# Performance work log

Hardware: AMD Instinct MI355X
Metric: run time of the kernel (lower is better)

The kernel has to match this reference:

```python
import jax, jax.numpy as jnp
import numpy as np

V, E, B, C = 10000, 128, 16, 128
N_REL = 8

def setup_inputs() -> dict:
    key = jax.random.key(0)
    k1, k2, k3, k4, k5 = jax.random.split(key, 5)
    src = jax.random.randint(k1, (B, C), 0, V, dtype=jnp.int32)
    src_embed = jax.random.normal(k2, (B, C, E), dtype=jnp.float32)
    embed_weight = jax.random.normal(k3, (V, E), dtype=jnp.float32)
    edge_matrix = jax.random.uniform(k4, (V, V), dtype=jnp.float32)
    relation_matrix = jax.random.randint(k5, (V, V), 0, 9, dtype=jnp.int32)
    return {"src": src, "src_embed": src_embed, "embed_weight": embed_weight,
            "edge_matrix": edge_matrix, "relation_matrix": relation_matrix}

def reference(src, src_embed, embed_weight, edge_matrix, relation_matrix):
    # base scores against full vocab: [B, C, V]
    base = jnp.einsum('bce,ve->bcv', src_embed, embed_weight)
    # gather the rows of both tables once: [B, C, V]
    edge_rows = edge_matrix[src]
    rel_rows = relation_matrix[src]
    concept_embeddings = []
    scores = []
    for i in range(N_REL):
        # ((relation_matrix == i+1) * edge_matrix)[src] > 0, gathered form
        mask = (jnp.where(rel_rows == i + 1, edge_rows, 0.0) > 0).astype(base.dtype)
        concept_weights = mask * base                     # [B, C, V]
        attn = jax.nn.softmax(concept_weights, axis=2)     # softmax over full vocab
        ce = jnp.einsum('bcv,ve->bce', attn, embed_weight) # [B, C, E]
        concept_embeddings.append(ce)
        scores.append(jnp.sum(src_embed * ce, axis=2, keepdims=True))
    scores = jnp.concatenate(scores, axis=2)               # [B, C, 8]
    weights = jax.nn.softmax(scores, axis=2)
    final = jnp.zeros_like(src_embed)
    for i in range(N_REL):
        final = final + weights[:, :, i:i + 1] * concept_embeddings[i]
    return final
```

## Files before the change

### kernel.cpp

```cpp
#include <hip/hip_runtime.h>

#define VV 10000
#define EE 128
#define NROWS 2048
#define KS 32

typedef unsigned short u16;
using short8 = __attribute__((ext_vector_type(8))) short;
using f32x4  = __attribute__((ext_vector_type(4))) float;

__device__ __forceinline__ u16 f2bf(float x) {
    unsigned u = __float_as_uint(x);
    return (u16)((u + 0x7fffu + ((u >> 16) & 1u)) >> 16);
}
__device__ __forceinline__ float bf2f(u16 h) {
    return __uint_as_float(((unsigned)h) << 16);
}

__global__ __launch_bounds__(256) void k0_prep(
    const float* __restrict__ SE,
    const float* __restrict__ W,
    u16* __restrict__ SEh, u16* __restrict__ SEl,
    u16* __restrict__ Wh,  u16* __restrict__ Wl,
    u16* __restrict__ WTh, u16* __restrict__ WTl)
{
    const int u = blockIdx.x * 256 + threadIdx.x;
    float x[8];
    u16 *dh, *dl;

    if (u < 32768) {
        int fid = u >> 6, l = u & 63;
        int nf = fid >> 2, kt = fid & 3;
        int row = nf * 16 + (l & 15);
        int k0 = kt * 32 + (l >> 4) * 8;
        const float* p = SE + row * EE + k0;
        float4 a = *(const float4*)p, b = *(const float4*)(p + 4);
        x[0]=a.x; x[1]=a.y; x[2]=a.z; x[3]=a.w;
        x[4]=b.x; x[5]=b.y; x[6]=b.z; x[7]=b.w;
        dh = SEh + u * 8; dl = SEl + u * 8;
    } else if (u < 192768) {
        int u2 = u - 32768;
        int fid = u2 >> 6, l = u2 & 63;
        int vf = fid >> 2, kt = fid & 3;
        int row = vf * 16 + (l & 15);
        int k0 = kt * 32 + (l >> 4) * 8;
        const float* p = W + row * EE + k0;
        float4 a = *(const float4*)p, b = *(const float4*)(p + 4);
        x[0]=a.x; x[1]=a.y; x[2]=a.z; x[3]=a.w;
        x[4]=b.x; x[5]=b.y; x[6]=b.z; x[7]=b.w;
        dh = Wh + u2 * 8; dl = Wl + u2 * 8;
    } else {
        int u3 = u - 192768;
        int fid = u3 >> 6, l = u3 & 63;
        int ef = fid / 313, kc = fid - ef * 313;
        int e  = ef * 16 + (l & 15);
        int k8 = kc * 32 + (l >> 4) * 8;
        if (k8 < VV) {
            #pragma unroll
            for (int i = 0; i < 8; i++) x[i] = W[(k8 + i) * EE + e];
        } else {
            #pragma unroll
            for (int i = 0; i < 8; i++) x[i] = 0.f;
        }
        dh = WTh + u3 * 8; dl = WTl + u3 * 8;
    }

    short8 hv, lv;
    #pragma unroll
    for (int i = 0; i < 8; i++) {
        u16 hb = f2bf(x[i]);
        hv[i] = (short)hb;
        lv[i] = (short)f2bf(x[i] - bf2f(hb));
    }
    *(short8*)dh = hv;
    *(short8*)dl = lv;
}

__global__ __launch_bounds__(256) void k1_mfma(
    const u16* __restrict__ SEh, const u16* __restrict__ SEl,
    const u16* __restrict__ Wh,  const u16* __restrict__ Wl,
    float* __restrict__ base)
{
    const int tid = threadIdx.x;
    const int l = tid & 63, wv = tid >> 6;
    const int wn = wv >> 1, wq = wv & 1;
    const int vt = blockIdx.x, nt = blockIdx.y;
    const int nf0 = nt * 4 + wn * 2;
    const int vf0 = vt * 8 + wq * 4;

    f32x4 acc[2][4];
    #pragma unroll
    for (int i = 0; i < 2; i++)
        #pragma unroll
        for (int j = 0; j < 4; j++)
            acc[i][j] = (f32x4){0.f, 0.f, 0.f, 0.f};

    #pragma unroll
    for (int kt = 0; kt < 4; ++kt) {
        short8 ah[2], al[2];
        #pragma unroll
        for (int i = 0; i < 2; ++i) {
            int off = (((nf0 + i) * 4 + kt) * 64 + l) * 8;
            ah[i] = *(const short8*)(SEh + off);
            al[i] = *(const short8*)(SEl + off);
        }
        #pragma unroll
        for (int j = 0; j < 4; ++j) {
            int vf = vf0 + j;
            short8 bh = {0,0,0,0,0,0,0,0};
            short8 bl = {0,0,0,0,0,0,0,0};
            if (vf < 625) {
                int off = ((vf * 4 + kt) * 64 + l) * 8;
                bh = *(const short8*)(Wh + off);
                bl = *(const short8*)(Wl + off);
            }
            #pragma unroll
            for (int i = 0; i < 2; ++i) {
                acc[i][j] = __builtin_amdgcn_mfma_f32_16x16x32_bf16(ah[i], bh, acc[i][j], 0, 0, 0);
                acc[i][j] = __builtin_amdgcn_mfma_f32_16x16x32_bf16(ah[i], bl, acc[i][j], 0, 0, 0);
                acc[i][j] = __builtin_amdgcn_mfma_f32_16x16x32_bf16(al[i], bh, acc[i][j], 0, 0, 0);
            }
        }
    }

    const int c = l & 15, r0 = (l >> 4) * 4;
    #pragma unroll
    for (int j = 0; j < 4; ++j) {
        int vf = vf0 + j;
        if (vf >= 625) continue;
        int v = vf * 16 + c;
        #pragma unroll
        for (int i = 0; i < 2; ++i) {
            int n = (nf0 + i) * 16 + r0;
            #pragma unroll
            for (int r = 0; r < 4; ++r)
                base[(n + r) * VV + v] = acc[i][j][r];
        }
    }
}

__global__ __launch_bounds__(256) void k2_stats(
    const int*   __restrict__ src,
    const float* __restrict__ edge,
    const int*   __restrict__ rel,
    float* __restrict__ baseA)
{
    __shared__ float seb[VV];
    __shared__ unsigned char srb[VV];
    __shared__ float wred[33][4];
    __shared__ float fin[33];
    __shared__ float cvals[12];

    const int n = blockIdx.x;
    const int tid = threadIdx.x;
    const int lane = tid & 63;
    const int wv = tid >> 6;
    const int s = src[n];
    const float4* brow4 = (const float4*)(baseA + (long long)n * VV);
    const float4* erow4 = (const float4*)(edge + (long long)s * VV);
    const int4*   rrow4 = (const int4*)(rel + (long long)s * VV);

    float accv[33];
    #pragma unroll
    for (int i = 0; i < 33; i++) accv[i] = 0.f;

    for (int v4 = tid; v4 < VV / 4; v4 += 256) {
        float4 b = brow4[v4];
        float4 e = erow4[v4];
        int4   r = rrow4[v4];
        float bb[4] = {b.x, b.y, b.z, b.w};
        float ee[4] = {e.x, e.y, e.z, e.w};
        int   rr[4] = {r.x, r.y, r.z, r.w};
        #pragma unroll
        for (int c = 0; c < 4; c++) {
            int rb = (rr[c] >= 1 && rr[c] <= 8 && ee[c] > 0.f) ? rr[c] : 0;
            float bc = bb[c];
            float eb = __expf(bc);
            float beb = bc * eb;
            seb[v4 * 4 + c] = eb;
            srb[v4 * 4 + c] = (unsigned char)rb;
            accv[0] += bc;
            #pragma unroll
            for (int q = 0; q < 8; q++) {
                float m = (rb == q + 1) ? 1.f : 0.f;
                accv[1 + q]  += m;
                accv[9 + q]  = fmaf(m, bc,  accv[9 + q]);
                accv[17 + q] = fmaf(m, eb,  accv[17 + q]);
                accv[25 + q] = fmaf(m, beb, accv[25 + q]);
            }
        }
    }

    #pragma unroll
    for (int i = 0; i < 33; i++) {
        float x = accv[i];
        #pragma unroll
        for (int off = 32; off > 0; off >>= 1) x += __shfl_xor(x, off, 64);
        if (lane == 0) wred[i][wv] = x;
    }
    __syncthreads();
    if (tid < 33)
        fin[tid] = wred[tid][0] + wred[tid][1] + wred[tid][2] + wred[tid][3];
    __syncthreads();

    if (tid == 0) {
        float sumbase = fin[0];
        float sc[8], Z[8];
        float smax = -1e30f;
        #pragma unroll
        for (int q = 0; q < 8; q++) {
            Z[q]  = ((float)VV - fin[1 + q]) + fin[17 + q];
            sc[q] = (sumbase - fin[9 + q] + fin[25 + q]) / Z[q];
            smax = fmaxf(smax, sc[q]);
        }
        float wsum = 0.f, wq[8];
        #pragma unroll
        for (int q = 0; q < 8; q++) { wq[q] = __expf(sc[q] - smax); wsum += wq[q]; }
        float Kc = 0.f;
        #pragma unroll
        for (int q = 0; q < 8; q++) {
            float c = (wq[q] / wsum) / Z[q];
            cvals[1 + q] = c;
            Kc += c;
        }
        cvals[0] = 0.f;
        cvals[9] = Kc;
    }
    __syncthreads();

    const float Kc = cvals[9];
    float4* broww = (float4*)(baseA + (long long)n * VV);
    for (int v4 = tid; v4 < VV / 4; v4 += 256) {
        float o[4];
        #pragma unroll
        for (int c = 0; c < 4; c++) {
            float eb = seb[v4 * 4 + c];
            float cc = cvals[srb[v4 * 4 + c]];
            o[c] = fmaf(cc, eb - 1.f, Kc);
        }
        broww[v4] = make_float4(o[0], o[1], o[2], o[3]);
    }
}

__global__ __launch_bounds__(256) void k3_mfma(
    const float* __restrict__ A,
    const u16* __restrict__ WTh, const u16* __restrict__ WTl,
    float* __restrict__ part)
{
    const int tid = threadIdx.x;
    const int l = tid & 63, wv = tid >> 6;
    const int mt = blockIdx.x, ks = blockIdx.y;
    const int mf0 = mt * 8 + wv * 2;
    const int g = l >> 4, rr_ = l & 15;

    f32x4 acc[2][8];
    #pragma unroll
    for (int i = 0; i < 2; i++)
        #pragma unroll
        for (int j = 0; j < 8; j++)
            acc[i][j] = (f32x4){0.f, 0.f, 0.f, 0.f};

    for (int kc = ks; kc < 313; kc += KS) {
        int k8 = kc * 32 + g * 8;
        short8 ah[2], al[2];
        #pragma unroll
        for (int i = 0; i < 2; ++i) {
            float x[8];
            if (k8 < VV) {
                const float* p = A + ((mf0 + i) * 16 + rr_) * VV + k8;
                float4 a = *(const float4*)p, b = *(const float4*)(p + 4);
                x[0]=a.x; x[1]=a.y; x[2]=a.z; x[3]=a.w;
                x[4]=b.x; x[5]=b.y; x[6]=b.z; x[7]=b.w;
            } else {
                #pragma unroll
                for (int q = 0; q < 8; q++) x[q] = 0.f;
            }
            #pragma unroll
            for (int q = 0; q < 8; q++) {
                u16 hb = f2bf(x[q]);
                ah[i][q] = (short)hb;
                al[i][q] = (short)f2bf(x[q] - bf2f(hb));
            }
        }
        #pragma unroll
        for (int j = 0; j < 8; ++j) {
            int off = ((j * 313 + kc) * 64 + l) * 8;
            short8 bh = *(const short8*)(WTh + off);
            short8 bl = *(const short8*)(WTl + off);
            #pragma unroll
            for (int i = 0; i < 2; ++i) {
                acc[i][j] = __builtin_amdgcn_mfma_f32_16x16x32_bf16(ah[i], bh, acc[i][j], 0, 0, 0);
                acc[i][j] = __builtin_amdgcn_mfma_f32_16x16x32_bf16(ah[i], bl, acc[i][j], 0, 0, 0);
                acc[i][j] = __builtin_amdgcn_mfma_f32_16x16x32_bf16(al[i], bh, acc[i][j], 0, 0, 0);
            }
        }
    }

    float* pp = part + (long long)ks * NROWS * EE;
    const int c = l & 15, r0 = g * 4;
    #pragma unroll
    for (int i = 0; i < 2; ++i) {
        #pragma unroll
        for (int j = 0; j < 8; ++j) {
            int e = j * 16 + c;
            int m = (mf0 + i) * 16 + r0;
            #pragma unroll
            for (int r = 0; r < 4; ++r)
                pp[(m + r) * EE + e] = acc[i][j][r];
        }
    }
}

__global__ __launch_bounds__(256) void k4_reduce(
    const float* __restrict__ part, float* __restrict__ out)
{
    int idx = blockIdx.x * 256 + threadIdx.x;
    const float4* p = (const float4*)part;
    const int stride = NROWS * EE / 4;
    float4 s = p[idx];
    #pragma unroll
    for (int k = 1; k < KS; k++) {
        float4 t = p[idx + k * stride];
        s.x += t.x; s.y += t.y; s.z += t.z; s.w += t.w;
    }
    ((float4*)out)[idx] = s;
}

extern "C" void kernel_launch(void* const* d_in, const int* in_sizes, int n_in,
                              void* d_out, int out_size, void* d_ws, size_t ws_size,
                              hipStream_t stream) {
    const int*   src  = (const int*)  d_in[0];
    const float* SE   = (const float*)d_in[1];
    const float* W    = (const float*)d_in[2];
    const float* edge = (const float*)d_in[3];
    const int*   rel  = (const int*)  d_in[4];
    float* out  = (float*)d_out;

    float* base = (float*)d_ws;
    float* part = base + (long long)NROWS * VV;
    u16* SEh = (u16*)(part + (long long)KS * NROWS * EE);
    u16* SEl = SEh + 262144;
    u16* Wh  = SEl + 262144;
    u16* Wl  = Wh  + 1280000;
    u16* WTh = Wl  + 1280000;
    u16* WTl = WTh + 1282048;

    k0_prep<<<dim3(1379), 256, 0, stream>>>(SE, W, SEh, SEl, Wh, Wl, WTh, WTl);
    k1_mfma<<<dim3(79, 32), 256, 0, stream>>>(SEh, SEl, Wh, Wl, base);
    k2_stats<<<dim3(NROWS), 256, 0, stream>>>(src, edge, rel, base);
    k3_mfma<<<dim3(16, KS), 256, 0, stream>>>(base, WTh, WTl, part);
    k4_reduce<<<dim3(256), 256, 0, stream>>>(part, out);
}
```

Baseline: 738.5 us.

## Keep stats row data in registers, contiguous K-split and retile matmul kernels

k2_stats stops staging exp values and relation bytes in about 50KB of shared memory. It keeps them in per-thread register arrays (packed relation codes) and adds a launch bound so more blocks can be resident. k3 now gives each wave one 16-row tile instead of two, doubling the grid. Each K-split also takes a contiguous chunk of k-steps instead of a strided one. k1 swaps grid axes so consecutive blocks share the same row tile and vary the vocab tile. The trade-offs are higher register pressure in k2 and less reuse of the W operand in k3.

```diff
diff --git a/kernel.cpp b/kernel.cpp
--- a/kernel.cpp
+++ b/kernel.cpp
@@ -84,7 +84,7 @@
     const int tid = threadIdx.x;
     const int l = tid & 63, wv = tid >> 6;
     const int wn = wv >> 1, wq = wv & 1;
-    const int vt = blockIdx.x, nt = blockIdx.y;
+    const int vt = blockIdx.y, nt = blockIdx.x;
     const int nf0 = nt * 4 + wn * 2;
     const int vf0 = vt * 8 + wq * 4;
 
@@ -139,14 +139,12 @@
     }
 }
 
-__global__ __launch_bounds__(256) void k2_stats(
+__global__ __launch_bounds__(256, 4) void k2_stats(
     const int*   __restrict__ src,
     const float* __restrict__ edge,
     const int*   __restrict__ rel,
     float* __restrict__ baseA)
 {
-    __shared__ float seb[VV];
-    __shared__ unsigned char srb[VV];
     __shared__ float wred[33][4];
     __shared__ float fin[33];
     __shared__ float cvals[12];
@@ -164,31 +162,43 @@
     #pragma unroll
     for (int i = 0; i < 33; i++) accv[i] = 0.f;
 
-    for (int v4 = tid; v4 < VV / 4; v4 += 256) {
-        float4 b = brow4[v4];
-        float4 e = erow4[v4];
-        int4   r = rrow4[v4];
-        float bb[4] = {b.x, b.y, b.z, b.w};
-        float ee[4] = {e.x, e.y, e.z, e.w};
-        int   rr[4] = {r.x, r.y, r.z, r.w};
-        #pragma unroll
-        for (int c = 0; c < 4; c++) {
-            int rb = (rr[c] >= 1 && rr[c] <= 8 && ee[c] > 0.f) ? rr[c] : 0;
-            float bc = bb[c];
-            float eb = __expf(bc);
-            float beb = bc * eb;
-            seb[v4 * 4 + c] = eb;
-            srb[v4 * 4 + c] = (unsigned char)rb;
-            accv[0] += bc;
-            #pragma unroll
-            for (int q = 0; q < 8; q++) {
-                float m = (rb == q + 1) ? 1.f : 0.f;
-                accv[1 + q]  += m;
-                accv[9 + q]  = fmaf(m, bc,  accv[9 + q]);
-                accv[17 + q] = fmaf(m, eb,  accv[17 + q]);
-                accv[25 + q] = fmaf(m, beb, accv[25 + q]);
-            }
-        }
+    float    ebr[10][4];
+    unsigned srp[10];
+
+    #pragma unroll
+    for (int it = 0; it < 10; ++it) {
+        int v4 = tid + it * 256;
+        unsigned pk = 0u;
+        if (v4 < VV / 4) {
+            float4 b = brow4[v4];
+            float4 e = erow4[v4];
+            int4   r = rrow4[v4];
+            float bb[4] = {b.x, b.y, b.z, b.w};
+            float ee[4] = {e.x, e.y, e.z, e.w};
+            int   rr[4] = {r.x, r.y, r.z, r.w};
+            #pragma unroll
+            for (int c = 0; c < 4; c++) {
+                int rb = (rr[c] >= 1 && rr[c] <= 8 && ee[c] > 0.f) ? rr[c] : 0;
+                float bc = bb[c];
+                float eb = __expf(bc);
+                float beb = bc * eb;
+                ebr[it][c] = eb;
+                pk |= ((unsigned)rb) << (8 * c);
+                accv[0] += bc;
+                #pragma unroll
+                for (int q = 0; q < 8; q++) {
+                    float m = (rb == q + 1) ? 1.f : 0.f;
+                    accv[1 + q]  += m;
+                    accv[9 + q]  = fmaf(m, bc,  accv[9 + q]);
+                    accv[17 + q] = fmaf(m, eb,  accv[17 + q]);
+                    accv[25 + q] = fmaf(m, beb, accv[25 + q]);
+                }
+            }
+        } else {
+            #pragma unroll
+            for (int c = 0; c < 4; c++) ebr[it][c] = 1.f;
+        }
+        srp[it] = pk;
     }
 
     #pragma unroll
@@ -230,15 +240,20 @@
 
     const float Kc = cvals[9];
     float4* broww = (float4*)(baseA + (long long)n * VV);
-    for (int v4 = tid; v4 < VV / 4; v4 += 256) {
-        float o[4];
-        #pragma unroll
-        for (int c = 0; c < 4; c++) {
-            float eb = seb[v4 * 4 + c];
-            float cc = cvals[srb[v4 * 4 + c]];
-            o[c] = fmaf(cc, eb - 1.f, Kc);
-        }
-        broww[v4] = make_float4(o[0], o[1], o[2], o[3]);
+    #pragma unroll
+    for (int it = 0; it < 10; ++it) {
+        int v4 = tid + it * 256;
+        if (v4 < VV / 4) {
+            unsigned pk = srp[it];
+            float o[4];
+            #pragma unroll
+            for (int c = 0; c < 4; c++) {
+                float eb = ebr[it][c];
+                float cc = cvals[(pk >> (8 * c)) & 255u];
+                o[c] = fmaf(cc, eb - 1.f, Kc);
+            }
+            broww[v4] = make_float4(o[0], o[1], o[2], o[3]);
+        }
     }
 }
 
@@ -250,24 +265,25 @@
     const int tid = threadIdx.x;
     const int l = tid & 63, wv = tid >> 6;
     const int mt = blockIdx.x, ks = blockIdx.y;
-    const int mf0 = mt * 8 + wv * 2;
+    const int mf = mt * 4 + wv;
     const int g = l >> 4, rr_ = l & 15;
-
-    f32x4 acc[2][8];
-    #pragma unroll
-    for (int i = 0; i < 2; i++)
-        #pragma unroll
-        for (int j = 0; j < 8; j++)
-            acc[i][j] = (f32x4){0.f, 0.f, 0.f, 0.f};
-
-    for (int kc = ks; kc < 313; kc += KS) {
+    const int kc0 = (313 * ks) / KS;
+    const int kc1 = (313 * (ks + 1)) / KS;
+
+    f32x4 acc[8];
+    #pragma unroll
+    for (int j = 0; j < 8; j++) acc[j] = (f32x4){0.f, 0.f, 0.f, 0.f};
+
+    const float* arow = A + (long long)(mf * 16 + rr_) * VV;
+
+    #pragma unroll 2
+    for (int kc = kc0; kc < kc1; ++kc) {
         int k8 = kc * 32 + g * 8;
-        short8 ah[2], al[2];
-        #pragma unroll
-        for (int i = 0; i < 2; ++i) {
+        short8 ah, al;
+        {
             float x[8];
             if (k8 < VV) {
-                const float* p = A + ((mf0 + i) * 16 + rr_) * VV + k8;
+                const float* p = arow + k8;
                 float4 a = *(const float4*)p, b = *(const float4*)(p + 4);
                 x[0]=a.x; x[1]=a.y; x[2]=a.z; x[3]=a.w;
                 x[4]=b.x; x[5]=b.y; x[6]=b.z; x[7]=b.w;
@@ -278,8 +294,8 @@
             #pragma unroll
             for (int q = 0; q < 8; q++) {
                 u16 hb = f2bf(x[q]);
-                ah[i][q] = (short)hb;
-                al[i][q] = (short)f2bf(x[q] - bf2f(hb));
+                ah[q] = (short)hb;
+                al[q] = (short)f2bf(x[q] - bf2f(hb));
             }
         }
         #pragma unroll
@@ -287,27 +303,21 @@
             int off = ((j * 313 + kc) * 64 + l) * 8;
             short8 bh = *(const short8*)(WTh + off);
             short8 bl = *(const short8*)(WTl + off);
-            #pragma unroll
-            for (int i = 0; i < 2; ++i) {
-                acc[i][j] = __builtin_amdgcn_mfma_f32_16x16x32_bf16(ah[i], bh, acc[i][j], 0, 0, 0);
-                acc[i][j] = __builtin_amdgcn_mfma_f32_16x16x32_bf16(ah[i], bl, acc[i][j], 0, 0, 0);
-                acc[i][j] = __builtin_amdgcn_mfma_f32_16x16x32_bf16(al[i], bh, acc[i][j], 0, 0, 0);
-            }
+            acc[j] = __builtin_amdgcn_mfma_f32_16x16x32_bf16(ah, bh, acc[j], 0, 0, 0);
+            acc[j] = __builtin_amdgcn_mfma_f32_16x16x32_bf16(ah, bl, acc[j], 0, 0, 0);
+            acc[j] = __builtin_amdgcn_mfma_f32_16x16x32_bf16(al, bh, acc[j], 0, 0, 0);
         }
     }
 
     float* pp = part + (long long)ks * NROWS * EE;
     const int c = l & 15, r0 = g * 4;
     #pragma unroll
-    for (int i = 0; i < 2; ++i) {
-        #pragma unroll
-        for (int j = 0; j < 8; ++j) {
-            int e = j * 16 + c;
-            int m = (mf0 + i) * 16 + r0;
-            #pragma unroll
-            for (int r = 0; r < 4; ++r)
-                pp[(m + r) * EE + e] = acc[i][j][r];
-        }
+    for (int j = 0; j < 8; ++j) {
+        int e = j * 16 + c;
+        int m = mf * 16 + r0;
+        #pragma unroll
+        for (int r = 0; r < 4; ++r)
+            pp[(m + r) * EE + e] = acc[j][r];
     }
 }
 
@@ -346,8 +356,8 @@
     u16* WTl = WTh + 1282048;
 
     k0_prep<<<dim3(1379), 256, 0, stream>>>(SE, W, SEh, SEl, Wh, Wl, WTh, WTl);
-    k1_mfma<<<dim3(79, 32), 256, 0, stream>>>(SEh, SEl, Wh, Wl, base);
+    k1_mfma<<<dim3(32, 79), 256, 0, stream>>>(SEh, SEl, Wh, Wl, base);
     k2_stats<<<dim3(NROWS), 256, 0, stream>>>(src, edge, rel, base);
-    k3_mfma<<<dim3(16, KS), 256, 0, stream>>>(base, WTh, WTl, part);
+    k3_mfma<<<dim3(32, KS), 256, 0, stream>>>(base, WTh, WTl, part);
     k4_reduce<<<dim3(256), 256, 0, stream>>>(part, out);
 }
```

After: 757.2 us. 2.5% more time.

## Fuse attention-weight construction into the second GEMM using packed relation codes

Applied to the files above, without the earlier changes.

k2 no longer writes the rewritten attention matrix back over base. It emits packed 4-bit relation codes per element plus 10 per-row coefficients, and k3 rebuilds the weights on the fly from base, exp, and a shared-memory coefficient lookup. This drops one full write and re-read of the 2048x10000 float matrix and frees about 50KB of shared memory in k2, at the cost of recomputing exp inside the GEMM loop. k3 is also retiled to 64 rows by 4 E-fragments per wave with contiguous K ranges per split, and k1's grid axes are swapped to change block ordering.

```diff
diff --git a/kernel.cpp b/kernel.cpp
--- a/kernel.cpp
+++ b/kernel.cpp
@@ -4,6 +4,7 @@
 #define EE 128
 #define NROWS 2048
 #define KS 32
+#define RBSTRIDE 5120
 
 typedef unsigned short u16;
 using short8 = __attribute__((ext_vector_type(8))) short;
@@ -84,7 +85,7 @@
     const int tid = threadIdx.x;
     const int l = tid & 63, wv = tid >> 6;
     const int wn = wv >> 1, wq = wv & 1;
-    const int vt = blockIdx.x, nt = blockIdx.y;
+    const int vt = blockIdx.y, nt = blockIdx.x;
     const int nf0 = nt * 4 + wn * 2;
     const int vf0 = vt * 8 + wq * 4;
 
@@ -143,13 +144,12 @@
     const int*   __restrict__ src,
     const float* __restrict__ edge,
     const int*   __restrict__ rel,
-    float* __restrict__ baseA)
-{
-    __shared__ float seb[VV];
-    __shared__ unsigned char srb[VV];
+    const float* __restrict__ baseA,
+    unsigned char* __restrict__ rb4,
+    float* __restrict__ cG)
+{
     __shared__ float wred[33][4];
     __shared__ float fin[33];
-    __shared__ float cvals[12];
 
     const int n = blockIdx.x;
     const int tid = threadIdx.x;
@@ -159,6 +159,7 @@
     const float4* brow4 = (const float4*)(baseA + (long long)n * VV);
     const float4* erow4 = (const float4*)(edge + (long long)s * VV);
     const int4*   rrow4 = (const int4*)(rel + (long long)s * VV);
+    unsigned short* crow = (unsigned short*)(rb4 + (long long)n * RBSTRIDE);
 
     float accv[33];
     #pragma unroll
@@ -171,14 +172,14 @@
         float bb[4] = {b.x, b.y, b.z, b.w};
         float ee[4] = {e.x, e.y, e.z, e.w};
         int   rr[4] = {r.x, r.y, r.z, r.w};
+        unsigned pk = 0u;
         #pragma unroll
         for (int c = 0; c < 4; c++) {
             int rb = (rr[c] >= 1 && rr[c] <= 8 && ee[c] > 0.f) ? rr[c] : 0;
             float bc = bb[c];
             float eb = __expf(bc);
             float beb = bc * eb;
-            seb[v4 * 4 + c] = eb;
-            srb[v4 * 4 + c] = (unsigned char)rb;
+            pk |= ((unsigned)rb) << (4 * c);
             accv[0] += bc;
             #pragma unroll
             for (int q = 0; q < 8; q++) {
@@ -189,6 +190,7 @@
                 accv[25 + q] = fmaf(m, beb, accv[25 + q]);
             }
         }
+        crow[v4] = (unsigned short)pk;
     }
 
     #pragma unroll
@@ -217,60 +219,77 @@
         #pragma unroll
         for (int q = 0; q < 8; q++) { wq[q] = __expf(sc[q] - smax); wsum += wq[q]; }
         float Kc = 0.f;
+        float* cg = cG + n * 10;
         #pragma unroll
         for (int q = 0; q < 8; q++) {
             float c = (wq[q] / wsum) / Z[q];
-            cvals[1 + q] = c;
+            cg[1 + q] = c;
             Kc += c;
         }
-        cvals[0] = 0.f;
-        cvals[9] = Kc;
-    }
-    __syncthreads();
-
-    const float Kc = cvals[9];
-    float4* broww = (float4*)(baseA + (long long)n * VV);
-    for (int v4 = tid; v4 < VV / 4; v4 += 256) {
-        float o[4];
-        #pragma unroll
-        for (int c = 0; c < 4; c++) {
-            float eb = seb[v4 * 4 + c];
-            float cc = cvals[srb[v4 * 4 + c]];
-            o[c] = fmaf(cc, eb - 1.f, Kc);
-        }
-        broww[v4] = make_float4(o[0], o[1], o[2], o[3]);
+        cg[0] = 0.f;
+        cg[9] = Kc;
     }
 }
 
 __global__ __launch_bounds__(256) void k3_mfma(
-    const float* __restrict__ A,
+    const float* __restrict__ baseA,
+    const unsigned char* __restrict__ rb4,
+    const float* __restrict__ cG,
     const u16* __restrict__ WTh, const u16* __restrict__ WTl,
     float* __restrict__ part)
 {
+    __shared__ float cvt[64][10];
+
     const int tid = threadIdx.x;
     const int l = tid & 63, wv = tid >> 6;
+    const int wm = wv >> 1, we = wv & 1;
     const int mt = blockIdx.x, ks = blockIdx.y;
-    const int mf0 = mt * 8 + wv * 2;
     const int g = l >> 4, rr_ = l & 15;
-
-    f32x4 acc[2][8];
+    const int kc0 = (313 * ks) / KS;
+    const int kc1 = (313 * (ks + 1)) / KS;
+
+    for (int t = tid; t < 640; t += 256)
+        cvt[t / 10][t % 10] = cG[(mt * 64 + t / 10) * 10 + (t % 10)];
+    __syncthreads();
+
+    const int mf0 = mt * 4 + wm * 2;
+    const int rl0 = (wm * 2) * 16 + rr_;
+    const int rl1 = (wm * 2 + 1) * 16 + rr_;
+    const float* arow0 = baseA + (long long)(mf0 * 16 + rr_) * VV;
+    const float* arow1 = baseA + (long long)((mf0 + 1) * 16 + rr_) * VV;
+    const unsigned char* rrow0 = rb4 + (long long)(mf0 * 16 + rr_) * RBSTRIDE;
+    const unsigned char* rrow1 = rb4 + (long long)((mf0 + 1) * 16 + rr_) * RBSTRIDE;
+    const float Kc0 = cvt[rl0][9];
+    const float Kc1 = cvt[rl1][9];
+
+    f32x4 acc[2][4];
     #pragma unroll
     for (int i = 0; i < 2; i++)
         #pragma unroll
-        for (int j = 0; j < 8; j++)
+        for (int j = 0; j < 4; j++)
             acc[i][j] = (f32x4){0.f, 0.f, 0.f, 0.f};
 
-    for (int kc = ks; kc < 313; kc += KS) {
+    for (int kc = kc0; kc < kc1; ++kc) {
         int k8 = kc * 32 + g * 8;
         short8 ah[2], al[2];
+
         #pragma unroll
         for (int i = 0; i < 2; ++i) {
+            const float* arow = i ? arow1 : arow0;
+            const unsigned char* rrow = i ? rrow1 : rrow0;
+            const float Kci = i ? Kc1 : Kc0;
+            const int rli = i ? rl1 : rl0;
             float x[8];
             if (k8 < VV) {
-                const float* p = A + ((mf0 + i) * 16 + rr_) * VV + k8;
-                float4 a = *(const float4*)p, b = *(const float4*)(p + 4);
-                x[0]=a.x; x[1]=a.y; x[2]=a.z; x[3]=a.w;
-                x[4]=b.x; x[5]=b.y; x[6]=b.z; x[7]=b.w;
+                float4 a = *(const float4*)(arow + k8);
+                float4 b = *(const float4*)(arow + k8 + 4);
+                unsigned cw = *(const unsigned*)(rrow + (k8 >> 1));
+                float t[8] = {a.x, a.y, a.z, a.w, b.x, b.y, b.z, b.w};
+                #pragma unroll
+                for (int q = 0; q < 8; q++) {
+                    float cc = cvt[rli][(cw >> (4 * q)) & 15u];
+                    x[q] = fmaf(cc, __expf(t[q]) - 1.f, Kci);
+                }
             } else {
                 #pragma unroll
                 for (int q = 0; q < 8; q++) x[q] = 0.f;
@@ -282,9 +301,11 @@
                 al[i][q] = (short)f2bf(x[q] - bf2f(hb));
             }
         }
-        #pragma unroll
-        for (int j = 0; j < 8; ++j) {
-            int off = ((j * 313 + kc) * 64 + l) * 8;
+
+        #pragma unroll
+        for (int j = 0; j < 4; ++j) {
+            int ef = we * 4 + j;
+            int off = ((ef * 313 + kc) * 64 + l) * 8;
             short8 bh = *(const short8*)(WTh + off);
             short8 bl = *(const short8*)(WTl + off);
             #pragma unroll
@@ -301,8 +322,8 @@
     #pragma unroll
     for (int i = 0; i < 2; ++i) {
         #pragma unroll
-        for (int j = 0; j < 8; ++j) {
-            int e = j * 16 + c;
+        for (int j = 0; j < 4; ++j) {
+            int e = (we * 4 + j) * 16 + c;
             int m = (mf0 + i) * 16 + r0;
             #pragma unroll
             for (int r = 0; r < 4; ++r)
@@ -344,10 +365,12 @@
     u16* Wl  = Wh  + 1280000;
     u16* WTh = Wl  + 1280000;
     u16* WTl = WTh + 1282048;
+    unsigned char* rb4 = (unsigned char*)(WTl + 1282048);
+    float* cG = (float*)(rb4 + (long long)NROWS * RBSTRIDE);
 
     k0_prep<<<dim3(1379), 256, 0, stream>>>(SE, W, SEh, SEl, Wh, Wl, WTh, WTl);
-    k1_mfma<<<dim3(79, 32), 256, 0, stream>>>(SEh, SEl, Wh, Wl, base);
-    k2_stats<<<dim3(NROWS), 256, 0, stream>>>(src, edge, rel, base);
-    k3_mfma<<<dim3(16, KS), 256, 0, stream>>>(base, WTh, WTl, part);
+    k1_mfma<<<dim3(32, 79), 256, 0, stream>>>(SEh, SEl, Wh, Wl, base);
+    k2_stats<<<dim3(NROWS), 256, 0, stream>>>(src, edge, rel, base, rb4, cG);
+    k3_mfma<<<dim3(32, KS), 256, 0, stream>>>(base, rb4, cG, WTh, WTl, part);
     k4_reduce<<<dim3(256), 256, 0, stream>>>(part, out);
 }
```

Measured after the change: 715.1 us. -3.2%, faster.
